# Performance work log

Measured on AMD Instinct MI355X. Metric: run time of the kernel, lower is better.

The kernel has to match this reference:

```python
import jax, jax.numpy as jnp
import numpy as np


def _cxcywh_to_xyxy(b):
    cx, cy, w, h = b[..., 0], b[..., 1], b[..., 2], b[..., 3]
    return jnp.stack([cx - 0.5 * w, cy - 0.5 * h, cx + 0.5 * w, cy + 0.5 * h], axis=-1)


def _generalized_box_iou(a, b):
    # a: [M,4] xyxy, b: [N,4] xyxy -> [M,N] GIoU matrix (DETR box_ops semantics)
    area_a = (a[:, 2] - a[:, 0]) * (a[:, 3] - a[:, 1])  # [M]
    area_b = (b[:, 2] - b[:, 0]) * (b[:, 3] - b[:, 1])  # [N]
    lt = jnp.maximum(a[:, None, :2], b[None, :, :2])    # [M,N,2]
    rb = jnp.minimum(a[:, None, 2:], b[None, :, 2:])
    wh = jnp.clip(rb - lt, 0.0)
    inter = wh[..., 0] * wh[..., 1]                     # [M,N]
    union = area_a[:, None] + area_b[None, :] - inter
    iou = inter / union
    lt_c = jnp.minimum(a[:, None, :2], b[None, :, :2])
    rb_c = jnp.maximum(a[:, None, 2:], b[None, :, 2:])
    wh_c = jnp.clip(rb_c - lt_c, 0.0)
    area_c = wh_c[..., 0] * wh_c[..., 1]
    return iou - (area_c - union) / area_c


def setup_inputs() -> dict:
    key = jax.random.key(0)
    k1, k2, k3 = jax.random.split(key, 3)
    B, T, N = 8, 64, 8
    # predicted boxes in cxcywh, all components in (0,1) -> positive w,h (valid)
    pred_boxes = jax.random.uniform(k1, (B, T, N, 4), dtype=jnp.float32)
    # target boxes directly in valid xyxy (code path uses them unconverted)
    centers = jax.random.uniform(k2, (B, T, N, 2), dtype=jnp.float32) * 0.8 + 0.1
    half_wh = (jax.random.uniform(k3, (B, T, N, 2), dtype=jnp.float32) * 0.2 + 0.02) * 0.5
    bboxes = jnp.concatenate([centers - half_wh, centers + half_wh], axis=-1)
    bboxes_mask = jnp.ones((B, T), dtype=bool)
    return {"pred_boxes": pred_boxes, "bboxes": bboxes, "bboxes_mask": bboxes_mask}


def reference(pred_boxes, bboxes, bboxes_mask):
    B, T, N, _ = pred_boxes.shape
    M = B * T * N
    # per-box validity (mask is per-frame, broadcast to boxes), as weights
    v = jnp.broadcast_to(bboxes_mask[:, :, None], (B, T, N)).reshape(M).astype(pred_boxes.dtype)
    src = _cxcywh_to_xyxy(pred_boxes.reshape(M, 4))   # [M,4]
    tgt = bboxes.reshape(M, 4)                        # [M,4]
    G = _generalized_box_iou(tgt, src)                # [M,M] rows=targets, cols=preds
    # argmax matching over valid prediction columns
    g_match = jnp.where(v[None, :] > 0, G, -jnp.inf)
    idx = jnp.argmax(g_match, axis=1)                 # [M]
    matched = src[idx]                                # [M,4]
    matched_gious = G[:, idx]                         # [M,M] (faithful to original)
    w = v[:, None] * v[idx][None, :]                  # validity weights
    loss_giou = 1.0 - jnp.sum(matched_gious * w) / jnp.sum(w)
    loss_bbox = jnp.sum(jnp.abs(matched - tgt) * v[:, None]) / (4.0 * jnp.sum(v))
    return loss_giou, loss_bbox
```

## Files before the change

### kernel.cpp

```cpp
#include <hip/hip_runtime.h>
#include <cmath>

#define WAVE 64
#define TPB  256
#define FTPB 1024

__device__ __forceinline__ float fastrcp(float x) { return __builtin_amdgcn_rcpf(x); }

__device__ __forceinline__ unsigned sortable_u32(float f) {
    unsigned b = __float_as_uint(f);
    return (b & 0x80000000u) ? ~b : (b | 0x80000000u);
}

__device__ __forceinline__ int mask_mode(const void* maskp) {
    const unsigned char* mb = (const unsigned char*)maskp;
    unsigned char b0 = mb[0], b1 = mb[1];
    if (b0 != 0 && b1 != 0) return 0;
    if (b0 != 0) return 1;
    return 2;
}
__device__ __forceinline__ float mask_v(const void* maskp, int t, int mode) {
    if (mode == 0) return ((const unsigned char*)maskp)[t] ? 1.0f : 0.0f;
    if (mode == 1) return ((const int*)maskp)[t] ? 1.0f : 0.0f;
    return (((const float*)maskp)[t] != 0.0f) ? 1.0f : 0.0f;
}
__device__ __forceinline__ int midx(int m, int nsh, int N) {
    return (nsh >= 0) ? (m >> nsh) : (m / N);
}

__global__ __launch_bounds__(TPB) void pass_kernel(
        const float4* __restrict__ pred, const float4* __restrict__ tgt,
        const void* __restrict__ maskp, int M, int nsh, int N,
        unsigned long long* __restrict__ keypart, float* __restrict__ colpart) {
    __shared__ float rowst[64][8];
    __shared__ float tr[4][8][65];

    const int mode = mask_mode(maskp);
    const int CR   = M >> 8;
    const int rg   = blockIdx.x / CR;
    const int cr   = blockIdx.x % CR;
    const int tid  = threadIdx.x;
    const int lane = tid & (WAVE - 1);
    const int warp = tid >> 6;
    const int i0   = rg * 64;

    if (tid < 64) {
        float4 t = tgt[i0 + tid];
        rowst[tid][0] = t.x; rowst[tid][1] = t.y;
        rowst[tid][2] = t.z; rowst[tid][3] = t.w;
        rowst[tid][4] = (t.z - t.x) * (t.w - t.y);
        rowst[tid][5] = mask_v(maskp, midx(i0 + tid, nsh, N), mode);
    }
    __syncthreads();

    const int c0 = (cr * 4 + warp) * 64;
    const int c  = c0 + lane;
    float4 p = pred[c];
    float bx1 = p.x - 0.5f * p.z, by1 = p.y - 0.5f * p.w;
    float bx2 = p.x + 0.5f * p.z, by2 = p.y + 0.5f * p.w;
    float aB  = (bx2 - bx1) * (by2 - by1);
    float vc  = mask_v(maskp, midx(c, nsh, N), mode);
    bool  mv  = vc > 0.0f;

    float colacc = 0.0f;
    float bestv[8];
    int   besti[8];
#pragma unroll
    for (int s = 0; s < 8; ++s) { bestv[s] = -INFINITY; besti[s] = 0; }

    const int rbase  = lane & 7;
    const int cslice = (lane >> 3) * 8;

#pragma unroll
    for (int s = 0; s < 8; ++s) {
#pragma unroll
        for (int r = 0; r < 8; ++r) {
            const int row = s * 8 + r;
            float ax1 = rowst[row][0], ay1 = rowst[row][1];
            float ax2 = rowst[row][2], ay2 = rowst[row][3];
            float aA  = rowst[row][4], vi = rowst[row][5];
            float ltx = fmaxf(ax1, bx1), lty = fmaxf(ay1, by1);
            float rbx = fminf(ax2, bx2), rby = fminf(ay2, by2);
            float w = fmaxf(rbx - ltx, 0.0f), h = fmaxf(rby - lty, 0.0f);
            float inter = w * h;
            float uni = aA + aB - inter;
            float cx1 = fminf(ax1, bx1), cy1 = fminf(ay1, by1);
            float cx2 = fmaxf(ax2, bx2), cy2 = fmaxf(ay2, by2);
            float areaC = (cx2 - cx1) * (cy2 - cy1);
            float hval = fmaf(uni, fastrcp(areaC), inter * fastrcp(uni));
            colacc = fmaf(vi, hval, colacc);
            tr[warp][r][lane] = mv ? hval : -INFINITY;
        }
#pragma unroll
        for (int j = 0; j < 8; ++j) {
            float val = tr[warp][rbase][cslice + j];
            int cidx = c0 + cslice + j;
            if (val > bestv[s]) { bestv[s] = val; besti[s] = cidx; }
        }
    }

#pragma unroll
    for (int s = 0; s < 8; ++s) {
        unsigned long long key = ((unsigned long long)sortable_u32(bestv[s]) << 32)
                               | (unsigned)(~besti[s]);
#pragma unroll
        for (int off = 8; off <= 32; off <<= 1) {
            unsigned long long ok = __shfl_xor(key, off);
            key = (ok > key) ? ok : key;
        }
        if (lane < 8)
            keypart[(size_t)(cr * 4 + warp) * M + (i0 + s * 8 + lane)] = key;
    }
    colpart[(size_t)rg * M + c] = colacc;
}

__global__ __launch_bounds__(TPB) void reduce_kernel(
        const unsigned long long* __restrict__ keypart,
        const float* __restrict__ colpart, int M, int P,
        int* __restrict__ idx, float* __restrict__ colsumh) {
    int m = blockIdx.x * blockDim.x + threadIdx.x;
    if (m >= M) return;
    unsigned long long k = keypart[m];
    for (int cc = 1; cc < P; ++cc) {
        unsigned long long kc = keypart[(size_t)cc * M + m];
        k = (kc > k) ? kc : k;
    }
    float s = colpart[m];
    for (int cc = 1; cc < P; ++cc) s += colpart[(size_t)cc * M + m];
    idx[m] = (int)(~(unsigned)k);
    colsumh[m] = s;
}

__device__ __forceinline__ double wave_sum_d(double x) {
    for (int off = 32; off >= 1; off >>= 1) x += __shfl_xor(x, off);
    return x;
}

__global__ __launch_bounds__(FTPB) void finalize_kernel(
        const float4* __restrict__ pred, const float4* __restrict__ tgt,
        const void* __restrict__ maskp, int M, int nsh, int N,
        const int* __restrict__ idx, const float* __restrict__ colsumh,
        float* __restrict__ out) {
    __shared__ double red[4 * (FTPB / WAVE)];
    const int mode = mask_mode(maskp);
    const int tid = threadIdx.x;

    double sumV = 0.0, S2 = 0.0, S1h = 0.0, bbox = 0.0;
    for (int m = tid; m < M; m += FTPB) {
        float vi = mask_v(maskp, midx(m, nsh, N), mode);
        int   k  = idx[m];
        float vk = mask_v(maskp, midx(k, nsh, N), mode);
        sumV += (double)vi;
        S2   += (double)vk;
        S1h  += (double)vk * (double)colsumh[k];
        float4 p = pred[k];
        float sx1 = p.x - 0.5f * p.z, sy1 = p.y - 0.5f * p.w;
        float sx2 = p.x + 0.5f * p.z, sy2 = p.y + 0.5f * p.w;
        float4 t = tgt[m];
        bbox += (double)vi * (double)(fabsf(sx1 - t.x) + fabsf(sy1 - t.y) +
                                      fabsf(sx2 - t.z) + fabsf(sy2 - t.w));
    }
    sumV = wave_sum_d(sumV);
    S2   = wave_sum_d(S2);
    S1h  = wave_sum_d(S1h);
    bbox = wave_sum_d(bbox);
    int wid = tid >> 6, lane = tid & (WAVE - 1);
    const int NW = FTPB / WAVE;
    if (lane == 0) {
        red[wid] = sumV; red[NW + wid] = S2; red[2 * NW + wid] = S1h; red[3 * NW + wid] = bbox;
    }
    __syncthreads();
    if (tid == 0) {
        double a = 0, b = 0, c = 0, d = 0;
        for (int w = 0; w < NW; ++w) {
            a += red[w]; b += red[NW + w]; c += red[2 * NW + w]; d += red[3 * NW + w];
        }
        out[0] = (float)(2.0 - c / (a * b));
        out[1] = (float)(d / (4.0 * a));
    }
}

extern "C" void kernel_launch(void* const* d_in, const int* in_sizes, int n_in,
                              void* d_out, int out_size, void* d_ws, size_t ws_size,
                              hipStream_t stream) {
    const float4* pred = (const float4*)d_in[0];
    const float4* tgt  = (const float4*)d_in[1];
    const void*   mask = d_in[2];

    int M = in_sizes[0] / 4;
    int N = M / in_sizes[2];
    int nsh = -1;
    for (int s = 0; s < 31; ++s) if ((1 << s) == N) { nsh = s; break; }

    int P = M / 64;

    char* ws = (char*)d_ws;
    unsigned long long* keypart = (unsigned long long*)ws; ws += (size_t)P * M * 8;
    float* colpart = (float*)ws;                           ws += (size_t)P * M * 4;
    int*   idx     = (int*)ws;                             ws += (size_t)M * 4;
    float* colsumh = (float*)ws;                           ws += (size_t)M * 4;
    float* out = (float*)d_out;

    int blocks = (M / 64) * (M / 256);
    pass_kernel<<<blocks, TPB, 0, stream>>>(pred, tgt, mask, M, nsh, N, keypart, colpart);

    reduce_kernel<<<(M + TPB - 1) / TPB, TPB, 0, stream>>>(keypart, colpart, M, P, idx, colsumh);

    finalize_kernel<<<1, FTPB, 0, stream>>>(pred, tgt, mask, M, nsh, N, idx, colsumh, out);
}
```

Baseline: 119.0 us.

## Replace partial-buffer reduction with atomics and precompute converted boxes

Adds a prep kernel that converts predictions to xyxy, precomputes areas and mask weights, and initializes accumulators. The pass kernel now has each wave handle a 64x64 tile. It merges row argmax keys with 64-bit atomicMax and column sums with float atomicAdd, which removes the large partial buffers and the separate reduce kernel. Column sums are now computed with a per-column wave shuffle reduction, which adds substantial ALU and shuffle work inside the inner loop. The float atomics also make the summation order nondeterministic.

Measured after the change: 95.53 us. -19.7%, faster.

```diff
diff --git a/kernel.cpp b/kernel.cpp
--- a/kernel.cpp
+++ b/kernel.cpp
@@ -4,6 +4,7 @@
 #define WAVE 64
 #define TPB  256
 #define FTPB 1024
+#define KEY_INIT 0x007FFFFFFFFFFFFFull
 
 __device__ __forceinline__ float fastrcp(float x) { return __builtin_amdgcn_rcpf(x); }
 
@@ -28,107 +29,80 @@
     return (nsh >= 0) ? (m >> nsh) : (m / N);
 }
 
-__global__ __launch_bounds__(TPB) void pass_kernel(
+__global__ __launch_bounds__(TPB) void prep_kernel(
         const float4* __restrict__ pred, const float4* __restrict__ tgt,
         const void* __restrict__ maskp, int M, int nsh, int N,
-        unsigned long long* __restrict__ keypart, float* __restrict__ colpart) {
-    __shared__ float rowst[64][8];
-    __shared__ float tr[4][8][65];
+        float4* __restrict__ convS, float* __restrict__ areaS,
+        float* __restrict__ areaT, float* __restrict__ vv,
+        unsigned long long* __restrict__ rowkey, float* __restrict__ colsumG) {
+    int m = blockIdx.x * blockDim.x + threadIdx.x;
+    if (m >= M) return;
+    float4 p = pred[m];
+    float x1 = p.x - 0.5f * p.z, y1 = p.y - 0.5f * p.w;
+    float x2 = p.x + 0.5f * p.z, y2 = p.y + 0.5f * p.w;
+    convS[m] = make_float4(x1, y1, x2, y2);
+    areaS[m] = (x2 - x1) * (y2 - y1);
+    float4 t = tgt[m];
+    areaT[m] = (t.z - t.x) * (t.w - t.y);
+    vv[m] = mask_v(maskp, midx(m, nsh, N), mask_mode(maskp));
+    rowkey[m] = KEY_INIT;
+    colsumG[m] = 0.0f;
+}
 
-    const int mode = mask_mode(maskp);
-    const int CR   = M >> 8;
-    const int rg   = blockIdx.x / CR;
-    const int cr   = blockIdx.x % CR;
-    const int tid  = threadIdx.x;
-    const int lane = tid & (WAVE - 1);
-    const int warp = tid >> 6;
-    const int i0   = rg * 64;
+__global__ __launch_bounds__(TPB) void pass_kernel(
+        const float4* __restrict__ tgt, const float* __restrict__ areaT,
+        const float4* __restrict__ convS, const float* __restrict__ areaS,
+        const float* __restrict__ vv, int M,
+        unsigned long long* __restrict__ rowkey, float* __restrict__ colsumG) {
+    const int CC   = M >> 6;
+    const int wid  = blockIdx.x * (TPB / WAVE) + (threadIdx.x >> 6);
+    const int lane = threadIdx.x & (WAVE - 1);
+    const int rb   = wid / CC;
+    const int cc   = wid % CC;
+    const int r    = rb * 64 + lane;
+    const int c0   = cc * 64;
 
-    if (tid < 64) {
-        float4 t = tgt[i0 + tid];
-        rowst[tid][0] = t.x; rowst[tid][1] = t.y;
-        rowst[tid][2] = t.z; rowst[tid][3] = t.w;
-        rowst[tid][4] = (t.z - t.x) * (t.w - t.y);
-        rowst[tid][5] = mask_v(maskp, midx(i0 + tid, nsh, N), mode);
-    }
-    __syncthreads();
+    float4 a  = tgt[r];
+    float  aA = areaT[r];
+    float  vi = vv[r];
 
-    const int c0 = (cr * 4 + warp) * 64;
-    const int c  = c0 + lane;
-    float4 p = pred[c];
-    float bx1 = p.x - 0.5f * p.z, by1 = p.y - 0.5f * p.w;
-    float bx2 = p.x + 0.5f * p.z, by2 = p.y + 0.5f * p.w;
-    float aB  = (bx2 - bx1) * (by2 - by1);
-    float vc  = mask_v(maskp, midx(c, nsh, N), mode);
-    bool  mv  = vc > 0.0f;
+    float vc = vv[c0 + lane];
+    unsigned long long cm = __ballot(vc > 0.0f);
 
-    float colacc = 0.0f;
-    float bestv[8];
-    int   besti[8];
-#pragma unroll
-    for (int s = 0; s < 8; ++s) { bestv[s] = -INFINITY; besti[s] = 0; }
+    float best = -INFINITY;
+    int   bidx = 0;
+    float csum = 0.0f;
 
-    const int rbase  = lane & 7;
-    const int cslice = (lane >> 3) * 8;
+    const float4* __restrict__ bcol = convS + c0;
+    const float*  __restrict__ bare = areaS + c0;
 
-#pragma unroll
-    for (int s = 0; s < 8; ++s) {
-#pragma unroll
-        for (int r = 0; r < 8; ++r) {
-            const int row = s * 8 + r;
-            float ax1 = rowst[row][0], ay1 = rowst[row][1];
-            float ax2 = rowst[row][2], ay2 = rowst[row][3];
-            float aA  = rowst[row][4], vi = rowst[row][5];
-            float ltx = fmaxf(ax1, bx1), lty = fmaxf(ay1, by1);
-            float rbx = fminf(ax2, bx2), rby = fminf(ay2, by2);
-            float w = fmaxf(rbx - ltx, 0.0f), h = fmaxf(rby - lty, 0.0f);
-            float inter = w * h;
-            float uni = aA + aB - inter;
-            float cx1 = fminf(ax1, bx1), cy1 = fminf(ay1, by1);
-            float cx2 = fmaxf(ax2, bx2), cy2 = fmaxf(ay2, by2);
-            float areaC = (cx2 - cx1) * (cy2 - cy1);
-            float hval = fmaf(uni, fastrcp(areaC), inter * fastrcp(uni));
-            colacc = fmaf(vi, hval, colacc);
-            tr[warp][r][lane] = mv ? hval : -INFINITY;
-        }
-#pragma unroll
-        for (int j = 0; j < 8; ++j) {
-            float val = tr[warp][rbase][cslice + j];
-            int cidx = c0 + cslice + j;
-            if (val > bestv[s]) { bestv[s] = val; besti[s] = cidx; }
+#pragma unroll 8
+    for (int j = 0; j < 64; ++j) {
+        float4 b  = bcol[j];
+        float  aB = bare[j];
+        float ltx = fmaxf(a.x, b.x), lty = fmaxf(a.y, b.y);
+        float rbx = fminf(a.z, b.z), rby = fminf(a.w, b.w);
+        float w = fmaxf(rbx - ltx, 0.0f), h = fmaxf(rby - lty, 0.0f);
+        float inter = w * h;
+        float uni = aA + aB - inter;
+        float cx1 = fminf(a.x, b.x), cy1 = fminf(a.y, b.y);
+        float cx2 = fmaxf(a.z, b.z), cy2 = fmaxf(a.w, b.w);
+        float areaC = (cx2 - cx1) * (cy2 - cy1);
+        float hval = fmaf(uni, fastrcp(areaC), inter * fastrcp(uni));
+
+        float t = vi * hval;
+        for (int off = 1; off <= 32; off <<= 1) t += __shfl_xor(t, off);
+        csum = (lane == j) ? t : csum;
+
+        if ((cm >> j) & 1ull) {
+            if (hval > best) { best = hval; bidx = c0 + j; }
         }
     }
 
-#pragma unroll
-    for (int s = 0; s < 8; ++s) {
-        unsigned long long key = ((unsigned long long)sortable_u32(bestv[s]) << 32)
-                               | (unsigned)(~besti[s]);
-#pragma unroll
-        for (int off = 8; off <= 32; off <<= 1) {
-            unsigned long long ok = __shfl_xor(key, off);
-            key = (ok > key) ? ok : key;
-        }
-        if (lane < 8)
-            keypart[(size_t)(cr * 4 + warp) * M + (i0 + s * 8 + lane)] = key;
-    }
-    colpart[(size_t)rg * M + c] = colacc;
-}
-
-__global__ __launch_bounds__(TPB) void reduce_kernel(
-        const unsigned long long* __restrict__ keypart,
-        const float* __restrict__ colpart, int M, int P,
-        int* __restrict__ idx, float* __restrict__ colsumh) {
-    int m = blockIdx.x * blockDim.x + threadIdx.x;
-    if (m >= M) return;
-    unsigned long long k = keypart[m];
-    for (int cc = 1; cc < P; ++cc) {
-        unsigned long long kc = keypart[(size_t)cc * M + m];
-        k = (kc > k) ? kc : k;
-    }
-    float s = colpart[m];
-    for (int cc = 1; cc < P; ++cc) s += colpart[(size_t)cc * M + m];
-    idx[m] = (int)(~(unsigned)k);
-    colsumh[m] = s;
+    unsigned long long key = ((unsigned long long)sortable_u32(best) << 32)
+                           | (unsigned)(~bidx);
+    atomicMax(&rowkey[r], key);
+    atomicAdd(&colsumG[c0 + lane], csum);
 }
 
 __device__ __forceinline__ double wave_sum_d(double x) {
@@ -137,28 +111,24 @@
 }
 
 __global__ __launch_bounds__(FTPB) void finalize_kernel(
-        const float4* __restrict__ pred, const float4* __restrict__ tgt,
-        const void* __restrict__ maskp, int M, int nsh, int N,
-        const int* __restrict__ idx, const float* __restrict__ colsumh,
-        float* __restrict__ out) {
+        const float4* __restrict__ convS, const float4* __restrict__ tgt,
+        const float* __restrict__ vv, const unsigned long long* __restrict__ rowkey,
+        const float* __restrict__ colsumG, int M, float* __restrict__ out) {
     __shared__ double red[4 * (FTPB / WAVE)];
-    const int mode = mask_mode(maskp);
     const int tid = threadIdx.x;
 
     double sumV = 0.0, S2 = 0.0, S1h = 0.0, bbox = 0.0;
     for (int m = tid; m < M; m += FTPB) {
-        float vi = mask_v(maskp, midx(m, nsh, N), mode);
-        int   k  = idx[m];
-        float vk = mask_v(maskp, midx(k, nsh, N), mode);
+        float vi = vv[m];
+        int   k  = (int)(~(unsigned)rowkey[m]);
+        float vk = vv[k];
         sumV += (double)vi;
         S2   += (double)vk;
-        S1h  += (double)vk * (double)colsumh[k];
-        float4 p = pred[k];
-        float sx1 = p.x - 0.5f * p.z, sy1 = p.y - 0.5f * p.w;
-        float sx2 = p.x + 0.5f * p.z, sy2 = p.y + 0.5f * p.w;
+        S1h  += (double)vk * (double)colsumG[k];
+        float4 s = convS[k];
         float4 t = tgt[m];
-        bbox += (double)vi * (double)(fabsf(sx1 - t.x) + fabsf(sy1 - t.y) +
-                                      fabsf(sx2 - t.z) + fabsf(sy2 - t.w));
+        bbox += (double)vi * (double)(fabsf(s.x - t.x) + fabsf(s.y - t.y) +
+                                      fabsf(s.z - t.z) + fabsf(s.w - t.w));
     }
     sumV = wave_sum_d(sumV);
     S2   = wave_sum_d(S2);
@@ -192,19 +162,22 @@
     int nsh = -1;
     for (int s = 0; s < 31; ++s) if ((1 << s) == N) { nsh = s; break; }
 
-    int P = M / 64;
+    char* ws = (char*)d_ws;
+    float4* convS   = (float4*)ws;             ws += (size_t)M * 16;
+    float*  areaS   = (float*)ws;              ws += (size_t)M * 4;
+    float*  areaT   = (float*)ws;              ws += (size_t)M * 4;
+    float*  vv      = (float*)ws;              ws += (size_t)M * 4;
+    unsigned long long* rowkey = (unsigned long long*)ws; ws += (size_t)M * 8;
+    float*  colsumG = (float*)ws;              ws += (size_t)M * 4;
+    float*  out = (float*)d_out;
 
-    char* ws = (char*)d_ws;
-    unsigned long long* keypart = (unsigned long long*)ws; ws += (size_t)P * M * 8;
-    float* colpart = (float*)ws;                           ws += (size_t)P * M * 4;
-    int*   idx     = (int*)ws;                             ws += (size_t)M * 4;
-    float* colsumh = (float*)ws;                           ws += (size_t)M * 4;
-    float* out = (float*)d_out;
+    prep_kernel<<<(M + TPB - 1) / TPB, TPB, 0, stream>>>(
+        pred, tgt, mask, M, nsh, N, convS, areaS, areaT, vv, rowkey, colsumG);
 
-    int blocks = (M / 64) * (M / 256);
-    pass_kernel<<<blocks, TPB, 0, stream>>>(pred, tgt, mask, M, nsh, N, keypart, colpart);
+    int waves  = (M / 64) * (M / 64);
+    int blocks = waves / (TPB / WAVE);
+    pass_kernel<<<blocks, TPB, 0, stream>>>(
+        tgt, areaT, convS, areaS, vv, M, rowkey, colsumG);
 
-    reduce_kernel<<<(M + TPB - 1) / TPB, TPB, 0, stream>>>(keypart, colpart, M, P, idx, colsumh);
-
-    finalize_kernel<<<1, FTPB, 0, stream>>>(pred, tgt, mask, M, nsh, N, idx, colsumh, out);
+    finalize_kernel<<<1, FTPB, 0, stream>>>(convS, tgt, vv, rowkey, colsumG, M, out);
 }
```
